# Kernel tuning notes

Hardware: AMD Instinct MI355X
Metric: run time of the kernel (lower is better)

Reference implementation:

```python
import jax, jax.numpy as jnp
import numpy as np


def setup_inputs() -> dict:
    key = jax.random.key(0)
    k1, k2, k3, k4, k5 = jax.random.split(key, 5)
    B, T, D, U = 64, 8192, 256, 128
    return {
        "target": jax.random.normal(k1, (B, T, D), dtype=jnp.float32),
        "source": jax.random.normal(k2, (B, D), dtype=jnp.float32),
        "W1": jax.random.normal(k3, (D, U), dtype=jnp.float32) * (1.0 / np.sqrt(D)),
        "W2": jax.random.normal(k4, (D, U), dtype=jnp.float32) * (1.0 / np.sqrt(D)),
        "attention_vals": jax.random.normal(k5, (U,), dtype=jnp.float32),
    }


def reference(target, source, W1, W2, attention_vals):
    # target: [B,T,D] -> w2 -> [B,T,U]; source: [B,D] -> w1 -> [B,1,U]
    t = jnp.einsum("btd,du->btu", target, W2)
    s = (source @ W1)[:, None, :]
    additive = jnp.tanh(s + t)                      # [B,T,U]
    scores = jnp.einsum("btu,u->bt", additive, attention_vals)  # [B,T]
    return scores
```

## Files before the change

kernel.cpp:

```cpp
#include <hip/hip_runtime.h>
#include <hip/hip_bf16.h>


#define B_ 64
#define T_ 8192
#define D_ 256
#define U_ 128
#define LDSW 264

typedef __attribute__((ext_vector_type(8))) short bf16x8;
typedef __attribute__((ext_vector_type(4))) float f32x4;

__device__ __forceinline__ short f2bf(float f) {
    unsigned u = __builtin_bit_cast(unsigned, f);
    u += 0x7fffu + ((u >> 16) & 1u);
    return (short)(u >> 16);
}

__device__ __forceinline__ float fast_tanh(float x) {
    float e = __expf(2.0f * x);
    return 1.0f - 2.0f * __builtin_amdgcn_rcpf(e + 1.0f);
}

__device__ __forceinline__ bf16x8 cvt8(const float4& a, const float4& b) {
    union { __hip_bfloat162 h[4]; bf16x8 v; } u;
    u.h[0] = __float22bfloat162_rn(make_float2(a.x, a.y));
    u.h[1] = __float22bfloat162_rn(make_float2(a.z, a.w));
    u.h[2] = __float22bfloat162_rn(make_float2(b.x, b.y));
    u.h[3] = __float22bfloat162_rn(make_float2(b.z, b.w));
    return u.v;
}

__global__ __launch_bounds__(512, 4) void additive_attn_kernel(
        const float* __restrict__ target,
        const float* __restrict__ source,
        const float* __restrict__ W1,
        const float* __restrict__ W2,
        const float* __restrict__ attn,
        float* __restrict__ out) {
    __shared__ __attribute__((aligned(16))) short lds_w2[U_ * LDSW];
    __shared__ float  lds_red[512];
    __shared__ float2 lds_sa[U_];

    const int tid = threadIdx.x;
    const int bx  = blockIdx.x;
    const int b   = bx >> 4;
    const int tb  = (bx & 15) << 9;

    const int lane = tid & 63;
    const int wave = tid >> 6;
    const int c = lane & 15;
    const int g = lane >> 4;

    const float* tgt  = target + ((size_t)b * T_ + tb) * D_;
    float*       outp = out + (size_t)b * T_ + tb;
    const float* Abase = tgt + (size_t)(wave * 16 + c) * D_ + g * 8;

    float4 xa0, xa1, xa2, xa3, xb0, xb1, xb2, xb3;

#define LOADB(X0, X1, X2, X3, BI) do {                                        \
    const float* p_ = Abase + (size_t)((BI) >> 2) * (128 * D_) + ((BI) & 3) * 64; \
    X0 = *(const float4*)(p_);      X1 = *(const float4*)(p_ + 4);            \
    X2 = *(const float4*)(p_ + 32); X3 = *(const float4*)(p_ + 36);           \
} while (0)

    LOADB(xa0, xa1, xa2, xa3, 0);

    {
        const int u    = tid & (U_ - 1);
        const int dblk = (tid >> 7) << 6;
        #pragma unroll
        for (int w = 0; w < 8; ++w) {
            const int d0 = dblk + w * 8;
            bf16x8 v;
            #pragma unroll
            for (int i = 0; i < 8; ++i)
                v[i] = f2bf(W2[(size_t)(d0 + i) * U_ + u]);
            *(bf16x8*)&lds_w2[u * LDSW + d0] = v;
        }
    }

    {
        const float* src = source + b * D_;
        const int u    = tid & (U_ - 1);
        const int part = tid >> 7;
        float acc = 0.f;
        #pragma unroll 8
        for (int d = part * 64; d < part * 64 + 64; ++d)
            acc = fmaf(src[d], W1[(size_t)d * U_ + u], acc);
        lds_red[tid] = acc;
    }
    __syncthreads();
    if (tid < U_)
        lds_sa[tid] = make_float2(
            lds_red[tid] + lds_red[tid + 128] + lds_red[tid + 256] + lds_red[tid + 384],
            attn[tid]);
    __syncthreads();

    f32x4 acc[8];
    #pragma unroll
    for (int j = 0; j < 8; ++j) acc[j] = (f32x4){0.f, 0.f, 0.f, 0.f};

#define COMP(X0, X1, X2, X3, Q) do {                                          \
    bf16x8 af0 = cvt8(X0, X1);                                                \
    bf16x8 af1 = cvt8(X2, X3);                                                \
    const int kb_ = (Q) * 64 + g * 8;                                         \
    _Pragma("unroll")                                                         \
    for (int j = 0; j < 8; ++j) {                                             \
        bf16x8 w0 = *(const bf16x8*)&lds_w2[(16 * j + c) * LDSW + kb_];       \
        acc[j] = __builtin_amdgcn_mfma_f32_16x16x32_bf16(w0, af0, acc[j], 0, 0, 0); \
        bf16x8 w1 = *(const bf16x8*)&lds_w2[(16 * j + c) * LDSW + kb_ + 32];  \
        acc[j] = __builtin_amdgcn_mfma_f32_16x16x32_bf16(w1, af1, acc[j], 0, 0, 0); \
    }                                                                         \
} while (0)

#define EPI(IT) do {                                                          \
    float sc = 0.f;                                                           \
    _Pragma("unroll")                                                         \
    for (int j = 0; j < 8; ++j) {                                             \
        float4 sa01 = *(const float4*)&lds_sa[16 * j + 4 * g];                \
        float4 sa23 = *(const float4*)&lds_sa[16 * j + 4 * g + 2];            \
        sc += fast_tanh(acc[j][0] + sa01.x) * sa01.y;                         \
        sc += fast_tanh(acc[j][1] + sa01.z) * sa01.w;                         \
        sc += fast_tanh(acc[j][2] + sa23.x) * sa23.y;                         \
        sc += fast_tanh(acc[j][3] + sa23.z) * sa23.w;                         \
        acc[j] = (f32x4){0.f, 0.f, 0.f, 0.f};                                 \
    }                                                                         \
    sc += __shfl_xor(sc, 16);                                                 \
    sc += __shfl_xor(sc, 32);                                                 \
    if (lane < 16) outp[(IT) * 128 + wave * 16 + lane] = sc;                  \
} while (0)

    #pragma unroll
    for (int bi = 0; bi < 16; ++bi) {
        if ((bi & 1) == 0) {
            if (bi < 15) LOADB(xb0, xb1, xb2, xb3, bi + 1);
            COMP(xa0, xa1, xa2, xa3, bi & 3);
        } else {
            if (bi < 15) LOADB(xa0, xa1, xa2, xa3, bi + 1);
            COMP(xb0, xb1, xb2, xb3, bi & 3);
        }
        if ((bi & 3) == 3) EPI(bi >> 2);
    }

#undef LOADB
#undef COMP
#undef EPI
}

extern "C" void kernel_launch(void* const* d_in, const int* in_sizes, int n_in,
                              void* d_out, int out_size, void* d_ws, size_t ws_size,
                              hipStream_t stream) {
    const float* target = (const float*)d_in[0];
    const float* source = (const float*)d_in[1];
    const float* W1     = (const float*)d_in[2];
    const float* W2     = (const float*)d_in[3];
    const float* attn   = (const float*)d_in[4];
    float* out = (float*)d_out;

    dim3 grid(B_ * (T_ / 512));
    dim3 block(512);
    hipLaunchKernelGGL(additive_attn_kernel, grid, block, 0, stream,
                       target, source, W1, W2, attn, out);
}
```

Before: 112.8 us.

## Split U across wave pairs and double rows per block with LDS reduction

Each block now covers 1024 timesteps with half as many blocks. Waves are paired so each handles half of the U outputs for a 16-row group, which halves accumulator registers. Partial scores are combined through LDS with a __syncthreads per 64-row step. The goal is to amortize the per-block W2 conversion and source projection over more rows and to lower register pressure. The cost is that each wave reloads the same target rows (each row is read by two waves) and a block-wide barrier is added every step. The double-buffered prefetch is replaced by a single register buffer, and the occupancy hint in launch_bounds is dropped.

```diff
diff --git a/kernel.cpp b/kernel.cpp
--- a/kernel.cpp
+++ b/kernel.cpp
@@ -31,7 +31,7 @@
     return u.v;
 }
 
-__global__ __launch_bounds__(512, 4) void additive_attn_kernel(
+__global__ __launch_bounds__(512) void additive_attn_kernel(
         const float* __restrict__ target,
         const float* __restrict__ source,
         const float* __restrict__ W1,
@@ -40,31 +40,35 @@
         float* __restrict__ out) {
     __shared__ __attribute__((aligned(16))) short lds_w2[U_ * LDSW];
     __shared__ float  lds_red[512];
-    __shared__ float2 lds_sa[U_];
+    __shared__ __attribute__((aligned(16))) float2 lds_sa[U_];
+    __shared__ float  lds_part[2][2][4][16];
 
-    const int tid = threadIdx.x;
-    const int bx  = blockIdx.x;
-    const int b   = bx >> 4;
-    const int tb  = (bx & 15) << 9;
+    const int tid  = threadIdx.x;
+    const int bx   = blockIdx.x;
+    const int b    = bx >> 3;
+    const int tb   = (bx & 7) << 10;
 
     const int lane = tid & 63;
     const int wave = tid >> 6;
-    const int c = lane & 15;
-    const int g = lane >> 4;
+    const int rg   = wave >> 1;
+    const int uh   = wave & 1;
+    const int c    = lane & 15;
+    const int g    = lane >> 4;
 
     const float* tgt  = target + ((size_t)b * T_ + tb) * D_;
     float*       outp = out + (size_t)b * T_ + tb;
-    const float* Abase = tgt + (size_t)(wave * 16 + c) * D_ + g * 8;
+    const float* Abase = tgt + (size_t)(rg * 16 + c) * D_ + g * 8;
+    const short* w2base = &lds_w2[(64 * uh + c) * LDSW];
 
-    float4 xa0, xa1, xa2, xa3, xb0, xb1, xb2, xb3;
+    float4 x0, x1, x2, x3;
 
-#define LOADB(X0, X1, X2, X3, BI) do {                                        \
-    const float* p_ = Abase + (size_t)((BI) >> 2) * (128 * D_) + ((BI) & 3) * 64; \
-    X0 = *(const float4*)(p_);      X1 = *(const float4*)(p_ + 4);            \
-    X2 = *(const float4*)(p_ + 32); X3 = *(const float4*)(p_ + 36);           \
+#define LOADQ(S, Q) do {                                                      \
+    const float* p_ = Abase + (size_t)(S) * (64 * D_) + (Q) * 64;             \
+    x0 = *(const float4*)(p_);      x1 = *(const float4*)(p_ + 4);            \
+    x2 = *(const float4*)(p_ + 32); x3 = *(const float4*)(p_ + 36);           \
 } while (0)
 
-    LOADB(xa0, xa1, xa2, xa3, 0);
+    LOADQ(0, 0);
 
     {
         const int u    = tid & (U_ - 1);
@@ -84,11 +88,11 @@
         const float* src = source + b * D_;
         const int u    = tid & (U_ - 1);
         const int part = tid >> 7;
-        float acc = 0.f;
+        float acc1 = 0.f;
         #pragma unroll 8
         for (int d = part * 64; d < part * 64 + 64; ++d)
-            acc = fmaf(src[d], W1[(size_t)d * U_ + u], acc);
-        lds_red[tid] = acc;
+            acc1 = fmaf(src[d], W1[(size_t)d * U_ + u], acc1);
+        lds_red[tid] = acc1;
     }
     __syncthreads();
     if (tid < U_)
@@ -97,55 +101,57 @@
             attn[tid]);
     __syncthreads();
 
-    f32x4 acc[8];
+    f32x4 acc[4];
     #pragma unroll
-    for (int j = 0; j < 8; ++j) acc[j] = (f32x4){0.f, 0.f, 0.f, 0.f};
+    for (int j = 0; j < 4; ++j) acc[j] = (f32x4){0.f, 0.f, 0.f, 0.f};
 
-#define COMP(X0, X1, X2, X3, Q) do {                                          \
-    bf16x8 af0 = cvt8(X0, X1);                                                \
-    bf16x8 af1 = cvt8(X2, X3);                                                \
+#define MFMAQ(AF0, AF1, Q) do {                                               \
     const int kb_ = (Q) * 64 + g * 8;                                         \
     _Pragma("unroll")                                                         \
-    for (int j = 0; j < 8; ++j) {                                             \
-        bf16x8 w0 = *(const bf16x8*)&lds_w2[(16 * j + c) * LDSW + kb_];       \
-        acc[j] = __builtin_amdgcn_mfma_f32_16x16x32_bf16(w0, af0, acc[j], 0, 0, 0); \
-        bf16x8 w1 = *(const bf16x8*)&lds_w2[(16 * j + c) * LDSW + kb_ + 32];  \
-        acc[j] = __builtin_amdgcn_mfma_f32_16x16x32_bf16(w1, af1, acc[j], 0, 0, 0); \
+    for (int j = 0; j < 4; ++j) {                                             \
+        bf16x8 w0 = *(const bf16x8*)(w2base + j * 16 * LDSW + kb_);           \
+        acc[j] = __builtin_amdgcn_mfma_f32_16x16x32_bf16(w0, AF0, acc[j], 0, 0, 0); \
+        bf16x8 w1 = *(const bf16x8*)(w2base + j * 16 * LDSW + kb_ + 32);      \
+        acc[j] = __builtin_amdgcn_mfma_f32_16x16x32_bf16(w1, AF1, acc[j], 0, 0, 0); \
     }                                                                         \
 } while (0)
 
-#define EPI(IT) do {                                                          \
-    float sc = 0.f;                                                           \
-    _Pragma("unroll")                                                         \
-    for (int j = 0; j < 8; ++j) {                                             \
-        float4 sa01 = *(const float4*)&lds_sa[16 * j + 4 * g];                \
-        float4 sa23 = *(const float4*)&lds_sa[16 * j + 4 * g + 2];            \
-        sc += fast_tanh(acc[j][0] + sa01.x) * sa01.y;                         \
-        sc += fast_tanh(acc[j][1] + sa01.z) * sa01.w;                         \
-        sc += fast_tanh(acc[j][2] + sa23.x) * sa23.y;                         \
-        sc += fast_tanh(acc[j][3] + sa23.z) * sa23.w;                         \
-        acc[j] = (f32x4){0.f, 0.f, 0.f, 0.f};                                 \
+#define STEP(S, Q) do {                                                       \
+    bf16x8 af0 = cvt8(x0, x1);                                                \
+    bf16x8 af1 = cvt8(x2, x3);                                                \
+    if (!((S) == 15 && (Q) == 3)) {                                           \
+        const int nx_ = (S) * 4 + (Q) + 1;                                    \
+        LOADQ(nx_ >> 2, nx_ & 3);                                             \
     }                                                                         \
-    sc += __shfl_xor(sc, 16);                                                 \
-    sc += __shfl_xor(sc, 32);                                                 \
-    if (lane < 16) outp[(IT) * 128 + wave * 16 + lane] = sc;                  \
+    MFMAQ(af0, af1, Q);                                                       \
 } while (0)
 
-    #pragma unroll
-    for (int bi = 0; bi < 16; ++bi) {
-        if ((bi & 1) == 0) {
-            if (bi < 15) LOADB(xb0, xb1, xb2, xb3, bi + 1);
-            COMP(xa0, xa1, xa2, xa3, bi & 3);
-        } else {
-            if (bi < 15) LOADB(xa0, xa1, xa2, xa3, bi + 1);
-            COMP(xb0, xb1, xb2, xb3, bi & 3);
+    for (int s = 0; s < 16; ++s) {
+        STEP(s, 0); STEP(s, 1); STEP(s, 2); STEP(s, 3);
+
+        float sc = 0.f;
+        #pragma unroll
+        for (int j = 0; j < 4; ++j) {
+            const float4 sa01 = *(const float4*)&lds_sa[uh * 64 + 16 * j + 4 * g];
+            const float4 sa23 = *(const float4*)&lds_sa[uh * 64 + 16 * j + 4 * g + 2];
+            sc += fast_tanh(acc[j][0] + sa01.x) * sa01.y;
+            sc += fast_tanh(acc[j][1] + sa01.z) * sa01.w;
+            sc += fast_tanh(acc[j][2] + sa23.x) * sa23.y;
+            sc += fast_tanh(acc[j][3] + sa23.z) * sa23.w;
+            acc[j] = (f32x4){0.f, 0.f, 0.f, 0.f};
         }
-        if ((bi & 3) == 3) EPI(bi >> 2);
+        sc += __shfl_xor(sc, 16);
+        sc += __shfl_xor(sc, 32);
+        if (lane < 16) lds_part[s & 1][uh][rg][lane] = sc;
+        __syncthreads();
+        if (tid < 64)
+            outp[s * 64 + tid] = lds_part[s & 1][0][tid >> 4][tid & 15]
+                               + lds_part[s & 1][1][tid >> 4][tid & 15];
     }
 
-#undef LOADB
-#undef COMP
-#undef EPI
+#undef LOADQ
+#undef MFMAQ
+#undef STEP
 }
 
 extern "C" void kernel_launch(void* const* d_in, const int* in_sizes, int n_in,
@@ -158,7 +164,7 @@
     const float* attn   = (const float*)d_in[4];
     float* out = (float*)d_out;
 
-    dim3 grid(B_ * (T_ / 512));
+    dim3 grid(B_ * (T_ / 1024));
     dim3 block(512);
     hipLaunchKernelGGL(additive_attn_kernel, grid, block, 0, stream,
                        target, source, W1, W2, attn, out);
```

Result: slower. 136.3 us (+20.8%).

## Double each block's row range and pipeline smaller per-step target loads

Applied to the files above, without the earlier changes.

Each block now covers 1024 time steps instead of 512, which halves the grid and halves how often W2 is converted to bf16 in LDS and W1·source is recomputed. The inner loop moves to 64 steps of 32-wide K chunks. Each step does two float4 loads per lane and prefetches two steps ahead, in place of four-float4 loads one step ahead. The occupancy hint on launch bounds is dropped. This cuts redundant per-block setup and register pressure, at the cost of fewer blocks and a smaller bytes-in-flight window per wave.

```diff
diff --git a/kernel.cpp b/kernel.cpp
--- a/kernel.cpp
+++ b/kernel.cpp
@@ -31,7 +31,7 @@
     return u.v;
 }
 
-__global__ __launch_bounds__(512, 4) void additive_attn_kernel(
+__global__ __launch_bounds__(512) void additive_attn_kernel(
         const float* __restrict__ target,
         const float* __restrict__ source,
         const float* __restrict__ W1,
@@ -40,31 +40,32 @@
         float* __restrict__ out) {
     __shared__ __attribute__((aligned(16))) short lds_w2[U_ * LDSW];
     __shared__ float  lds_red[512];
-    __shared__ float2 lds_sa[U_];
+    __shared__ __attribute__((aligned(16))) float2 lds_sa[U_];
 
-    const int tid = threadIdx.x;
-    const int bx  = blockIdx.x;
-    const int b   = bx >> 4;
-    const int tb  = (bx & 15) << 9;
+    const int tid  = threadIdx.x;
+    const int bx   = blockIdx.x;
+    const int b    = bx >> 3;
+    const int tb   = (bx & 7) << 10;
 
     const int lane = tid & 63;
     const int wave = tid >> 6;
-    const int c = lane & 15;
-    const int g = lane >> 4;
+    const int c    = lane & 15;
+    const int g    = lane >> 4;
 
     const float* tgt  = target + ((size_t)b * T_ + tb) * D_;
     float*       outp = out + (size_t)b * T_ + tb;
     const float* Abase = tgt + (size_t)(wave * 16 + c) * D_ + g * 8;
 
-    float4 xa0, xa1, xa2, xa3, xb0, xb1, xb2, xb3;
+    float4 xa0, xa1, xb0, xb1;
 
-#define LOADB(X0, X1, X2, X3, BI) do {                                        \
-    const float* p_ = Abase + (size_t)((BI) >> 2) * (128 * D_) + ((BI) & 3) * 64; \
-    X0 = *(const float4*)(p_);      X1 = *(const float4*)(p_ + 4);            \
-    X2 = *(const float4*)(p_ + 32); X3 = *(const float4*)(p_ + 36);           \
+#define LOADE(X0, X1, S) do {                                                 \
+    const float* p_ = Abase + (size_t)((S) >> 3) * (128 * D_) + ((S) & 7) * 32; \
+    X0 = *(const float4*)(p_);                                                \
+    X1 = *(const float4*)(p_ + 4);                                            \
 } while (0)
 
-    LOADB(xa0, xa1, xa2, xa3, 0);
+    LOADE(xa0, xa1, 0);
+    LOADE(xb0, xb1, 1);
 
     {
         const int u    = tid & (U_ - 1);
@@ -84,11 +85,11 @@
         const float* src = source + b * D_;
         const int u    = tid & (U_ - 1);
         const int part = tid >> 7;
-        float acc = 0.f;
+        float a1 = 0.f;
         #pragma unroll 8
         for (int d = part * 64; d < part * 64 + 64; ++d)
-            acc = fmaf(src[d], W1[(size_t)d * U_ + u], acc);
-        lds_red[tid] = acc;
+            a1 = fmaf(src[d], W1[(size_t)d * U_ + u], a1);
+        lds_red[tid] = a1;
     }
     __syncthreads();
     if (tid < U_)
@@ -101,25 +102,12 @@
     #pragma unroll
     for (int j = 0; j < 8; ++j) acc[j] = (f32x4){0.f, 0.f, 0.f, 0.f};
 
-#define COMP(X0, X1, X2, X3, Q) do {                                          \
-    bf16x8 af0 = cvt8(X0, X1);                                                \
-    bf16x8 af1 = cvt8(X2, X3);                                                \
-    const int kb_ = (Q) * 64 + g * 8;                                         \
-    _Pragma("unroll")                                                         \
-    for (int j = 0; j < 8; ++j) {                                             \
-        bf16x8 w0 = *(const bf16x8*)&lds_w2[(16 * j + c) * LDSW + kb_];       \
-        acc[j] = __builtin_amdgcn_mfma_f32_16x16x32_bf16(w0, af0, acc[j], 0, 0, 0); \
-        bf16x8 w1 = *(const bf16x8*)&lds_w2[(16 * j + c) * LDSW + kb_ + 32];  \
-        acc[j] = __builtin_amdgcn_mfma_f32_16x16x32_bf16(w1, af1, acc[j], 0, 0, 0); \
-    }                                                                         \
-} while (0)
-
-#define EPI(IT) do {                                                          \
+#define EPI(RT) do {                                                          \
     float sc = 0.f;                                                           \
     _Pragma("unroll")                                                         \
     for (int j = 0; j < 8; ++j) {                                             \
-        float4 sa01 = *(const float4*)&lds_sa[16 * j + 4 * g];                \
-        float4 sa23 = *(const float4*)&lds_sa[16 * j + 4 * g + 2];            \
+        const float4 sa01 = *(const float4*)&lds_sa[16 * j + 4 * g];          \
+        const float4 sa23 = *(const float4*)&lds_sa[16 * j + 4 * g + 2];      \
         sc += fast_tanh(acc[j][0] + sa01.x) * sa01.y;                         \
         sc += fast_tanh(acc[j][1] + sa01.z) * sa01.w;                         \
         sc += fast_tanh(acc[j][2] + sa23.x) * sa23.y;                         \
@@ -128,23 +116,29 @@
     }                                                                         \
     sc += __shfl_xor(sc, 16);                                                 \
     sc += __shfl_xor(sc, 32);                                                 \
-    if (lane < 16) outp[(IT) * 128 + wave * 16 + lane] = sc;                  \
+    if (lane < 16) outp[(RT) * 128 + wave * 16 + lane] = sc;                  \
 } while (0)
 
     #pragma unroll
-    for (int bi = 0; bi < 16; ++bi) {
-        if ((bi & 1) == 0) {
-            if (bi < 15) LOADB(xb0, xb1, xb2, xb3, bi + 1);
-            COMP(xa0, xa1, xa2, xa3, bi & 3);
+    for (int s = 0; s < 64; ++s) {
+        bf16x8 af;
+        if ((s & 1) == 0) {
+            af = cvt8(xa0, xa1);
+            if (s < 62) LOADE(xa0, xa1, s + 2);
         } else {
-            if (bi < 15) LOADB(xa0, xa1, xa2, xa3, bi + 1);
-            COMP(xb0, xb1, xb2, xb3, bi & 3);
+            af = cvt8(xb0, xb1);
+            if (s < 62) LOADE(xb0, xb1, s + 2);
         }
-        if ((bi & 3) == 3) EPI(bi >> 2);
+        const int kb = (s & 7) * 32 + g * 8;
+        #pragma unroll
+        for (int j = 0; j < 8; ++j) {
+            bf16x8 wfj = *(const bf16x8*)&lds_w2[(16 * j + c) * LDSW + kb];
+            acc[j] = __builtin_amdgcn_mfma_f32_16x16x32_bf16(wfj, af, acc[j], 0, 0, 0);
+        }
+        if ((s & 7) == 7) EPI(s >> 3);
     }
 
-#undef LOADB
-#undef COMP
+#undef LOADE
 #undef EPI
 }
 
@@ -158,7 +152,7 @@
     const float* attn   = (const float*)d_in[4];
     float* out = (float*)d_out;
 
-    dim3 grid(B_ * (T_ / 512));
+    dim3 grid(B_ * (T_ / 1024));
     dim3 block(512);
     hipLaunchKernelGGL(additive_attn_kernel, grid, block, 0, stream,
                        target, source, W1, W2, attn, out);
```

Result: slower. 417.0 us (+269.7%).
